# Kernel tuning notes

Hardware: AMD Instinct MI355X
Metric: run time of the kernel (lower is better)

Reference implementation:

```python
import jax, jax.numpy as jnp
import numpy as np

N = 100000   # nodes
E = 1600000  # edges (avg degree 16)
F_IN = 50    # dataset.num_features
C = 32       # dataset.num_classes == hidden == out channels


def setup_inputs() -> dict:
    key = jax.random.key(0)
    ks = jax.random.split(key, 12)
    x = jax.random.normal(ks[0], (N, F_IN), dtype=jnp.float32)
    edge_index = jax.random.randint(ks[1], (2, E), 0, N, dtype=jnp.int64)
    dims = [(F_IN, C), (C, C), (C, C)]
    inp = {"x": x, "edge_index": edge_index}
    for i, (din, dout) in enumerate(dims, start=1):
        s = 1.0 / np.sqrt(din)
        inp[f"Wl{i}"] = jax.random.uniform(ks[2 + 3 * (i - 1)], (din, dout), jnp.float32, -s, s)
        inp[f"bl{i}"] = jax.random.uniform(ks[3 + 3 * (i - 1)], (dout,), jnp.float32, -s, s)
        inp[f"Wr{i}"] = jax.random.uniform(ks[4 + 3 * (i - 1)], (din, dout), jnp.float32, -s, s)
    return inp


def _sage_conv(x, src, dst, Wl, bl, Wr):
    # message = x[src]; scatter-max into dst; lin_l(agg) + lin_r(x)
    msg = x[src]                                      # [E, d_in]
    agg = jax.ops.segment_max(msg, dst, num_segments=N)
    agg = jnp.where(jnp.isfinite(agg), agg, jnp.zeros((), agg.dtype))  # empty segments -> 0
    return agg @ Wl + bl + x @ Wr


def reference(x, edge_index, Wl1, bl1, Wr1, Wl2, bl2, Wr2, Wl3, bl3, Wr3):
    src, dst = edge_index[0], edge_index[1]
    h = jax.nn.relu(_sage_conv(x, src, dst, Wl1, bl1, Wr1))
    h = jax.nn.relu(_sage_conv(h, src, dst, Wl2, bl2, Wr2))
    h = _sage_conv(h, src, dst, Wl3, bl3, Wr3)
    return jax.nn.log_softmax(h, axis=1)
```

## Files before the change

### kernel.cpp

```cpp
#include <hip/hip_runtime.h>
#include <math.h>

#define NN 100000
#define CD 32
#define NPB 4

#define B1N ((NN + 255) >> 8)
#define EPB_A 2048

typedef unsigned int   uint32;
typedef unsigned short ushort16;

__device__ __forceinline__ ushort16 f2b(float f) {
    uint32 u = __float_as_uint(f);
    u = (u + 0x7FFFu + ((u >> 16) & 1u)) >> 16;
    return (ushort16)u;
}
__device__ __forceinline__ float b2f_lo(uint32 u) { return __uint_as_float(u << 16); }
__device__ __forceinline__ float b2f_hi(uint32 u) { return __uint_as_float(u & 0xFFFF0000u); }

__device__ __forceinline__ uint32 pkmax(uint32 a, uint32 b) {
    uint32 d;
    asm("v_pk_max_u16 %0, %1, %2" : "=v"(d) : "v"(a), "v"(b));
    return d;
}
__device__ __forceinline__ uint32 key16(float f) {
    uint32 b = (uint32)f2b(f);
    return b ^ ((__float_as_uint(f) >> 31) ? 0xFFFFu : 0x8000u);
}
__device__ __forceinline__ uint32 dec_pk(uint32 k) {
    uint32 m = (~k >> 15) & 0x00010001u;
    uint32 X = 0x80008000u | ((m << 15) - m);
    return k ^ X;
}

__device__ __forceinline__ int edge_is64(const void* edge) {
    const long long* p = (const long long*)edge;
    int lane = threadIdx.x & 63;
    int bad = 0;
    for (int i = lane; i < 512; i += 64) {
        long long v = p[i];
        if (v < 0 || v >= NN) bad = 1;
    }
    unsigned long long anybad = __ballot(bad);
    return (anybad == 0ULL) ? 1 : 0;
}

__device__ __forceinline__ int load_idx(const void* edge, int i, int is64) {
    if (is64) return (int)((const long long*)edge)[i];
    return ((const int*)edge)[i];
}

__global__ __launch_bounds__(256) void cvt_hist_kernel(const float* __restrict__ x,
                                                       uint32* __restrict__ xb,
                                                       const void* edge, int E,
                                                       int* __restrict__ hist,
                                                       int nblkA) {
    __shared__ int lh[B1N];
    const int t = threadIdx.x;
    if ((int)blockIdx.x < nblkA) {
        const int is64 = edge_is64(edge);
        for (int b = t; b < B1N; b += 256) lh[b] = 0;
        __syncthreads();
        const int e0 = blockIdx.x * EPB_A + t;
#pragma unroll
        for (int k = 0; k < 8; ++k) {
            int e = e0 + k * 256;
            if (e < E) {
                int d = load_idx(edge, E + e, is64);
                atomicAdd(&lh[d >> 8], 1);
            }
        }
        __syncthreads();
        int* gh = hist + (size_t)blockIdx.x * B1N;
        for (int b = t; b < B1N; b += 256) gh[b] = lh[b];
    } else {
        const int tt = (blockIdx.x - nblkA) * 256 + t;
        if (tt >= NN * 32) return;
        const int n = tt >> 5;
        const int c = tt & 31;
        if (c >= 25) { xb[tt] = 0; return; }
        float2 v = *(const float2*)&x[n * 50 + 2 * c];
        xb[tt] = key16(v.x) | (key16(v.y) << 16);
    }
}

__global__ __launch_bounds__(256) void scanA_kernel(int* __restrict__ hist,
                                                    int nblk,
                                                    int* __restrict__ binTotal) {
    __shared__ int ts[256];
    const int bin = blockIdx.x;
    const int t = threadIdx.x;
    const int base = t * 4;
    int v0 = (base + 0 < nblk) ? hist[(size_t)(base + 0) * B1N + bin] : 0;
    int v1 = (base + 1 < nblk) ? hist[(size_t)(base + 1) * B1N + bin] : 0;
    int v2 = (base + 2 < nblk) ? hist[(size_t)(base + 2) * B1N + bin] : 0;
    int v3 = (base + 3 < nblk) ? hist[(size_t)(base + 3) * B1N + bin] : 0;
    const int s = v0 + v1 + v2 + v3;
    ts[t] = s;
    __syncthreads();
    for (int off = 1; off < 256; off <<= 1) {
        int u = (t >= off) ? ts[t - off] : 0;
        __syncthreads();
        ts[t] += u;
        __syncthreads();
    }
    int e = ts[t] - s;
    if (base + 0 < nblk) { hist[(size_t)(base + 0) * B1N + bin] = e; e += v0; }
    if (base + 1 < nblk) { hist[(size_t)(base + 1) * B1N + bin] = e; e += v1; }
    if (base + 2 < nblk) { hist[(size_t)(base + 2) * B1N + bin] = e; e += v2; }
    if (base + 3 < nblk) { hist[(size_t)(base + 3) * B1N + bin] = e; e += v3; }
    if (t == 255) binTotal[bin] = ts[255];
}

__device__ __forceinline__ void scan_bins_lds(const int* __restrict__ binTotal,
                                              int* ts, int* lbase) {
    const int t = threadIdx.x;
    const int base = t * 2;
    const int v0 = (base + 0 < B1N) ? binTotal[base + 0] : 0;
    const int v1 = (base + 1 < B1N) ? binTotal[base + 1] : 0;
    const int s = v0 + v1;
    ts[t] = s;
    __syncthreads();
    for (int off = 1; off < 256; off <<= 1) {
        int u = (t >= off) ? ts[t - off] : 0;
        __syncthreads();
        ts[t] += u;
        __syncthreads();
    }
    const int e = ts[t] - s;
    if (base + 0 < B1N) lbase[base + 0] = e;
    if (base + 1 < B1N) lbase[base + 1] = e + v0;
    if (t == 255) lbase[B1N] = ts[255];
    __syncthreads();
}

__global__ __launch_bounds__(256) void scatter_kernel(const void* edge, int E,
                                                      const int* __restrict__ hist,
                                                      const int* __restrict__ binTotal,
                                                      uint32* __restrict__ bucketed) {
    __shared__ int ts[256];
    __shared__ int lbase[B1N + 1];
    __shared__ int cur[B1N];
    const int is64 = edge_is64(edge);
    const int t = threadIdx.x;
    scan_bins_lds(binTotal, ts, lbase);
    const int* gh = hist + (size_t)blockIdx.x * B1N;
    for (int b = t; b < B1N; b += 256) cur[b] = lbase[b] + gh[b];
    __syncthreads();
    const int e0 = blockIdx.x * EPB_A + t;
#pragma unroll
    for (int k = 0; k < 8; ++k) {
        int e = e0 + k * 256;
        if (e < E) {
            int s = load_idx(edge, e, is64);
            int d = load_idx(edge, E + e, is64);
            int pos = atomicAdd(&cur[d >> 8], 1);
            bucketed[pos] = (uint32)s | ((uint32)(d & 255) << 17);
        }
    }
}

__global__ __launch_bounds__(256) void bucket_kernel(const uint32* __restrict__ bucketed,
                                                     const int* __restrict__ binTotal,
                                                     int* __restrict__ offsets,
                                                     int* __restrict__ csr_src) {
    __shared__ int ts[256];
    __shared__ int lbase[B1N + 1];
    __shared__ int h[256];
    __shared__ int sc[256];
    __shared__ int cur[256];
    const int bkt = blockIdx.x;
    const int t = threadIdx.x;
    scan_bins_lds(binTotal, ts, lbase);
    const int start = lbase[bkt];
    const int end   = lbase[bkt + 1];
    h[t] = 0;
    __syncthreads();
    for (int i = start + t; i < end; i += 256)
        atomicAdd(&h[bucketed[i] >> 17], 1);
    __syncthreads();
    const int v = h[t];
    sc[t] = v;
    __syncthreads();
    for (int off = 1; off < 256; off <<= 1) {
        int u = (t >= off) ? sc[t - off] : 0;
        __syncthreads();
        sc[t] += u;
        __syncthreads();
    }
    const int excl = sc[t] - v;
    const int node = bkt * 256 + t;
    if (node < NN) offsets[node] = start + excl;
    cur[t] = start + excl;
    __syncthreads();
    for (int i = start + t; i < end; i += 256) {
        uint32 p = bucketed[i];
        int pos = atomicAdd(&cur[p >> 17], 1);
        csr_src[pos] = (int)(p & 0x1FFFFu);
    }
    if (bkt == B1N - 1 && t == 0) offsets[NN] = end;
}


__device__ __forceinline__ void g50_window(uint32* a_, int sidx, int mm,
                                           const char* hbase, uint32 joff,
                                           int p, int lb) {
    int k = p;
    for (; k + 14 < mm; k += 16) {
        const int kh = lb + (k >> 1);
#pragma unroll
        for (int kk = 0; kk < 8; ++kk) {
            int s = __shfl(sidx, kh + kk);
            uint32 u = *(const uint32*)(hbase + ((((uint32)s) << 7) | joff));
            a_[kk] = pkmax(a_[kk], u);
        }
    }
    for (; k + 6 < mm; k += 8) {
        const int kh = lb + (k >> 1);
#pragma unroll
        for (int kk = 0; kk < 4; ++kk) {
            int s = __shfl(sidx, kh + kk);
            uint32 u = *(const uint32*)(hbase + ((((uint32)s) << 7) | joff));
            a_[kk] = pkmax(a_[kk], u);
        }
    }
    for (; k < mm; k += 2) {
        int s = __shfl(sidx, lb + (k >> 1));
        uint32 u = *(const uint32*)(hbase + ((((uint32)s) << 7) | joff));
        a_[0] = pkmax(a_[0], u);
    }
}

__global__ void gather50_kernel(const uint32* __restrict__ hb,
                                const int* __restrict__ offsets,
                                const int* __restrict__ csr_src,
                                uint32* __restrict__ aggB) {
    const int tid  = threadIdx.x;
    const int g    = tid >> 6;
    const int lane = tid & 63;
    const int p    = lane >> 5;
    const int j    = lane & 31;
    const int n0   = (blockIdx.x * NPB + g) * 2;
    if (n0 >= NN) return;
    const int n1   = n0 + 1;
    const bool has1 = (n1 < NN);

    const int beg0 = offsets[n0];
    const int end0 = offsets[n0 + 1];
    const int beg1 = has1 ? offsets[n1] : 0;
    const int end1 = has1 ? offsets[n1 + 1] : 0;
    const char* hbase = (const char*)hb;
    const uint32 joff = (uint32)(j << 2);
    const int lb = p << 5;
    const int myidx = 2 * j + p;

    uint32 a_[8], b_[8];
#pragma unroll
    for (int k = 0; k < 8; ++k) { a_[k] = 0; b_[k] = 0; }

    const int d0 = end0 - beg0, d1 = end1 - beg1;
    const int mm0 = d0 < 64 ? d0 : 64;
    const int mm1 = d1 < 64 ? d1 : 64;
    int sidx0 = 0, sidx1 = 0;
    if (myidx < mm0) sidx0 = csr_src[beg0 + myidx];
    if (myidx < mm1) sidx1 = csr_src[beg1 + myidx];
    g50_window(a_, sidx0, mm0, hbase, joff, p, lb);
    g50_window(b_, sidx1, mm1, hbase, joff, p, lb);
    for (int ib = beg0 + 64; ib < end0; ib += 64) {
        const int rem = end0 - ib;
        const int mm = rem < 64 ? rem : 64;
        int s = (myidx < mm) ? csr_src[ib + myidx] : 0;
        g50_window(a_, s, mm, hbase, joff, p, lb);
    }
    for (int ib = beg1 + 64; ib < end1; ib += 64) {
        const int rem = end1 - ib;
        const int mm = rem < 64 ? rem : 64;
        int s = (myidx < mm) ? csr_src[ib + myidx] : 0;
        g50_window(b_, s, mm, hbase, joff, p, lb);
    }

#pragma unroll
    for (int off2 = 4; off2 > 0; off2 >>= 1)
#pragma unroll
        for (int k = 0; k < off2; ++k) {
            a_[k] = pkmax(a_[k], a_[k + off2]);
            b_[k] = pkmax(b_[k], b_[k + off2]);
        }
    uint32 r0 = a_[0], r1 = b_[0];
    r0 = pkmax(r0, (uint32)__shfl_xor((int)r0, 32));
    r1 = pkmax(r1, (uint32)__shfl_xor((int)r1, 32));
    if (p == 0 && j < 25) {
        aggB[(size_t)n0 * 32 + j] = (beg0 == end0) ? 0x80008000u : r0;
        if (has1)
            aggB[(size_t)n1 * 32 + j] = (beg1 == end1) ? 0x80008000u : r1;
    }
}

__device__ __forceinline__ void g32_window(uint32* a_, int sidx, int mm,
                                           const char* hbase, uint32 coff,
                                           int e, int lb) {
    int k = e;
    for (; k + 12 < mm; k += 16) {
        const int m = lb + (k >> 2);
        int s0 = __shfl(sidx, m);
        int s1 = __shfl(sidx, m + 1);
        int s2 = __shfl(sidx, m + 2);
        int s3 = __shfl(sidx, m + 3);
        uint32 u0 = *(const uint32*)(hbase + ((((uint32)s0) << 6) | coff));
        uint32 u1 = *(const uint32*)(hbase + ((((uint32)s1) << 6) | coff));
        uint32 u2 = *(const uint32*)(hbase + ((((uint32)s2) << 6) | coff));
        uint32 u3 = *(const uint32*)(hbase + ((((uint32)s3) << 6) | coff));
        a_[0] = pkmax(a_[0], u0); a_[1] = pkmax(a_[1], u1);
        a_[2] = pkmax(a_[2], u2); a_[3] = pkmax(a_[3], u3);
    }
    for (; k < mm; k += 4) {
        int s = __shfl(sidx, lb + (k >> 2));
        uint32 u = *(const uint32*)(hbase + ((((uint32)s) << 6) | coff));
        a_[0] = pkmax(a_[0], u);
    }
}

__global__ void gather32_kernel(const uint32* __restrict__ hb,
                                const int* __restrict__ offsets,
                                const int* __restrict__ csr_src,
                                uint32* __restrict__ aggB) {
    const int tid  = threadIdx.x;
    const int g    = tid >> 6;
    const int lane = tid & 63;
    const int e    = lane >> 4;
    const int c    = lane & 15;
    const int n0   = (blockIdx.x * NPB + g) * 2;
    if (n0 >= NN) return;
    const int n1   = n0 + 1;
    const bool has1 = (n1 < NN);

    const int beg0 = offsets[n0];
    const int end0 = offsets[n0 + 1];
    const int beg1 = has1 ? offsets[n1] : 0;
    const int end1 = has1 ? offsets[n1 + 1] : 0;
    const char* hbase = (const char*)hb;
    const uint32 coff = (uint32)(c << 2);
    const int lb = e << 4;
    const int myidx = 4 * c + e;

    uint32 a_[4] = {0, 0, 0, 0};
    uint32 b_[4] = {0, 0, 0, 0};

    const int d0 = end0 - beg0, d1 = end1 - beg1;
    const int mm0 = d0 < 64 ? d0 : 64;
    const int mm1 = d1 < 64 ? d1 : 64;
    int sidx0 = 0, sidx1 = 0;
    if (myidx < mm0) sidx0 = csr_src[beg0 + myidx];
    if (myidx < mm1) sidx1 = csr_src[beg1 + myidx];
    g32_window(a_, sidx0, mm0, hbase, coff, e, lb);
    g32_window(b_, sidx1, mm1, hbase, coff, e, lb);
    for (int ib = beg0 + 64; ib < end0; ib += 64) {
        const int rem = end0 - ib;
        const int mm = rem < 64 ? rem : 64;
        int s = (myidx < mm) ? csr_src[ib + myidx] : 0;
        g32_window(a_, s, mm, hbase, coff, e, lb);
    }
    for (int ib = beg1 + 64; ib < end1; ib += 64) {
        const int rem = end1 - ib;
        const int mm = rem < 64 ? rem : 64;
        int s = (myidx < mm) ? csr_src[ib + myidx] : 0;
        g32_window(b_, s, mm, hbase, coff, e, lb);
    }

    uint32 r0 = pkmax(pkmax(a_[0], a_[1]), pkmax(a_[2], a_[3]));
    uint32 r1 = pkmax(pkmax(b_[0], b_[1]), pkmax(b_[2], b_[3]));
    r0 = pkmax(r0, (uint32)__shfl_xor((int)r0, 16));
    r0 = pkmax(r0, (uint32)__shfl_xor((int)r0, 32));
    r1 = pkmax(r1, (uint32)__shfl_xor((int)r1, 16));
    r1 = pkmax(r1, (uint32)__shfl_xor((int)r1, 32));
    if (lane < 16) {
        aggB[(size_t)n0 * 16 + lane] = (beg0 == end0) ? 0x80008000u : r0;
        if (has1)
            aggB[(size_t)n1 * 16 + lane] = (beg1 == end1) ? 0x80008000u : r1;
    }
}

template <int DIN, int ASTR, int HSTR, int OSTR, int MODE>
__global__ void dense_kernel(const uint32* __restrict__ aggB,
                             const uint32* __restrict__ hB,
                             const float* __restrict__ Wl,
                             const float* __restrict__ bl,
                             const float* __restrict__ Wr,
                             void* __restrict__ out_v) {
    const int n = blockIdx.x * blockDim.x + threadIdx.x;
    if (n >= NN) return;

    float acc[CD];
#pragma unroll
    for (int j = 0; j < CD; ++j) acc[j] = bl[j];

    {
        const uint32* row = aggB + (size_t)n * ASTR;
        for (int c = 0; c < DIN / 4; ++c) {
            uint2 u = *(const uint2*)&row[c * 2];
            u.x = dec_pk(u.x); u.y = dec_pk(u.y);
            float d0 = b2f_lo(u.x), d1 = b2f_hi(u.x);
            float d2 = b2f_lo(u.y), d3 = b2f_hi(u.y);
            const float* w = Wl + c * 4 * CD;
#pragma unroll
            for (int j = 0; j < CD; ++j)
                acc[j] += d0 * w[j] + d1 * w[CD + j] + d2 * w[2 * CD + j] + d3 * w[3 * CD + j];
        }
        if (DIN % 4) {
            uint32 u = dec_pk(row[(DIN / 4) * 2]);
            float d0 = b2f_lo(u), d1 = b2f_hi(u);
            const float* w = Wl + (DIN - 2) * CD;
#pragma unroll
            for (int j = 0; j < CD; ++j)
                acc[j] += d0 * w[j] + d1 * w[CD + j];
        }
    }
    {
        const uint32* row = hB + (size_t)n * HSTR;
        for (int c = 0; c < DIN / 4; ++c) {
            uint2 u = *(const uint2*)&row[c * 2];
            u.x = dec_pk(u.x); u.y = dec_pk(u.y);
            float d0 = b2f_lo(u.x), d1 = b2f_hi(u.x);
            float d2 = b2f_lo(u.y), d3 = b2f_hi(u.y);
            const float* w = Wr + c * 4 * CD;
#pragma unroll
            for (int j = 0; j < CD; ++j)
                acc[j] += d0 * w[j] + d1 * w[CD + j] + d2 * w[2 * CD + j] + d3 * w[3 * CD + j];
        }
        if (DIN % 4) {
            uint32 u = dec_pk(row[(DIN / 4) * 2]);
            float d0 = b2f_lo(u), d1 = b2f_hi(u);
            const float* w = Wr + (DIN - 2) * CD;
#pragma unroll
            for (int j = 0; j < CD; ++j)
                acc[j] += d0 * w[j] + d1 * w[CD + j];
        }
    }

    if (MODE == 0) {
        uint32* orow = (uint32*)out_v + (size_t)n * OSTR;
#pragma unroll
        for (int c = 0; c < CD / 2; ++c) {
            float a0 = fmaxf(acc[2 * c],     0.0f);
            float a1 = fmaxf(acc[2 * c + 1], 0.0f);
            orow[c] = ((uint32)f2b(a0) | ((uint32)f2b(a1) << 16)) | 0x80008000u;
        }
    } else {
        float m = acc[0];
#pragma unroll
        for (int j = 1; j < CD; ++j) m = fmaxf(m, acc[j]);
        float s = 0.0f;
#pragma unroll
        for (int j = 0; j < CD; ++j) s += expf(acc[j] - m);
        const float lse = m + logf(s);
        float* orow = (float*)out_v + (size_t)n * CD;
#pragma unroll
        for (int j = 0; j < CD; ++j) orow[j] = acc[j] - lse;
    }
}

extern "C" void kernel_launch(void* const* d_in, const int* in_sizes, int n_in,
                              void* d_out, int out_size, void* d_ws, size_t ws_size,
                              hipStream_t stream) {
    const float* x    = (const float*)d_in[0];
    const void*  edge = d_in[1];
    const float* Wl1 = (const float*)d_in[2];
    const float* bl1 = (const float*)d_in[3];
    const float* Wr1 = (const float*)d_in[4];
    const float* Wl2 = (const float*)d_in[5];
    const float* bl2 = (const float*)d_in[6];
    const float* Wr2 = (const float*)d_in[7];
    const float* Wl3 = (const float*)d_in[8];
    const float* bl3 = (const float*)d_in[9];
    const float* Wr3 = (const float*)d_in[10];

    const int E = in_sizes[1] / 2;

    char* ws = (char*)d_ws;
    size_t off = 0;
    auto carve = [&](size_t bytes) {
        void* p = ws + off;
        off = (off + bytes + 255) & ~(size_t)255;
        return p;
    };
    int*    offsets   = (int*)   carve((size_t)(NN + 1) * 4);
    int*    binTotal  = (int*)   carve((size_t)B1N * 4);
    int*    csr_src   = (int*)   carve((size_t)E * 4);
    uint32* xb        = (uint32*)carve((size_t)NN * 32 * 4);
    uint32* h1b       = (uint32*)carve((size_t)NN * 16 * 4);
    (void)ws_size; (void)n_in; (void)out_size;

    uint32* bucketed = (uint32*)d_out;
    int*    hist     = (int*)((char*)d_out + (((size_t)E * 4 + 255) & ~(size_t)255));
    uint32* agg1 = (uint32*)d_out;
    uint32* agg2 = (uint32*)d_out;
    uint32* h2b  = xb;
    uint32* agg3 = h1b;

    const int nblkA = (E + EPB_A - 1) / EPB_A;
    const int cvtb  = (NN * 32 + 255) / 256;
    cvt_hist_kernel<<<nblkA + cvtb, 256, 0, stream>>>(x, xb, edge, E, hist, nblkA);
    scanA_kernel<<<B1N, 256, 0, stream>>>(hist, nblkA, binTotal);
    scatter_kernel<<<nblkA, 256, 0, stream>>>(edge, E, hist, binTotal, bucketed);
    bucket_kernel<<<B1N, 256, 0, stream>>>(bucketed, binTotal, offsets, csr_src);

    const int gb = (NN + NPB * 2 - 1) / (NPB * 2);
    const int db = (NN + 255) / 256;

    gather50_kernel<<<gb, 256, 0, stream>>>(xb, offsets, csr_src, agg1);
    dense_kernel<50, 32, 32, 16, 0><<<db, 256, 0, stream>>>(agg1, xb, Wl1, bl1, Wr1, h1b);
    gather32_kernel<<<gb, 256, 0, stream>>>(h1b, offsets, csr_src, agg2);
    dense_kernel<32, 16, 16, 16, 0><<<db, 256, 0, stream>>>(agg2, h1b, Wl2, bl2, Wr2, h2b);
    gather32_kernel<<<gb, 256, 0, stream>>>(h2b, offsets, csr_src, agg3);
    dense_kernel<32, 16, 16, 0, 2><<<db, 256, 0, stream>>>(agg3, h2b, Wl3, bl3, Wr3, d_out);
}
```

Measured before the change: 289.2 us.

## Fuse all stages into one persistent cooperative kernel with grid syncs

Replaces the ten separate kernel launches (histogram, scans, scatter, bucket, three gather and three dense stages) with one cooperative persistent kernel. Each stage loops over virtual blocks and stages are separated by grid.sync(). The goal is to remove launch gaps and inter-kernel drain/fill bubbles. The cost is grid-sync overhead, occupancy reduced by the combined LDS and register footprint, and grid-stride looping that may load-balance worse than native launches.

```diff
diff --git a/kernel.cpp b/kernel.cpp
--- a/kernel.cpp
+++ b/kernel.cpp
@@ -1,9 +1,13 @@
 #include <hip/hip_runtime.h>
+#include <hip/hip_cooperative_groups.h>
 #include <math.h>
+
+namespace cg = cooperative_groups;
 
 #define NN 100000
 #define CD 32
 #define NPB 4
+#define G_NPW 2
 
 #define B1N ((NN + 255) >> 8)
 #define EPB_A 2048
@@ -51,157 +55,17 @@
     return ((const int*)edge)[i];
 }
 
-__global__ __launch_bounds__(256) void cvt_hist_kernel(const float* __restrict__ x,
-                                                       uint32* __restrict__ xb,
-                                                       const void* edge, int E,
-                                                       int* __restrict__ hist,
-                                                       int nblkA) {
-    __shared__ int lh[B1N];
-    const int t = threadIdx.x;
-    if ((int)blockIdx.x < nblkA) {
-        const int is64 = edge_is64(edge);
-        for (int b = t; b < B1N; b += 256) lh[b] = 0;
-        __syncthreads();
-        const int e0 = blockIdx.x * EPB_A + t;
-#pragma unroll
-        for (int k = 0; k < 8; ++k) {
-            int e = e0 + k * 256;
-            if (e < E) {
-                int d = load_idx(edge, E + e, is64);
-                atomicAdd(&lh[d >> 8], 1);
-            }
-        }
-        __syncthreads();
-        int* gh = hist + (size_t)blockIdx.x * B1N;
-        for (int b = t; b < B1N; b += 256) gh[b] = lh[b];
-    } else {
-        const int tt = (blockIdx.x - nblkA) * 256 + t;
-        if (tt >= NN * 32) return;
-        const int n = tt >> 5;
-        const int c = tt & 31;
-        if (c >= 25) { xb[tt] = 0; return; }
-        float2 v = *(const float2*)&x[n * 50 + 2 * c];
-        xb[tt] = key16(v.x) | (key16(v.y) << 16);
-    }
-}
-
-__global__ __launch_bounds__(256) void scanA_kernel(int* __restrict__ hist,
-                                                    int nblk,
-                                                    int* __restrict__ binTotal) {
-    __shared__ int ts[256];
-    const int bin = blockIdx.x;
-    const int t = threadIdx.x;
-    const int base = t * 4;
-    int v0 = (base + 0 < nblk) ? hist[(size_t)(base + 0) * B1N + bin] : 0;
-    int v1 = (base + 1 < nblk) ? hist[(size_t)(base + 1) * B1N + bin] : 0;
-    int v2 = (base + 2 < nblk) ? hist[(size_t)(base + 2) * B1N + bin] : 0;
-    int v3 = (base + 3 < nblk) ? hist[(size_t)(base + 3) * B1N + bin] : 0;
-    const int s = v0 + v1 + v2 + v3;
-    ts[t] = s;
-    __syncthreads();
-    for (int off = 1; off < 256; off <<= 1) {
-        int u = (t >= off) ? ts[t - off] : 0;
-        __syncthreads();
-        ts[t] += u;
-        __syncthreads();
-    }
-    int e = ts[t] - s;
-    if (base + 0 < nblk) { hist[(size_t)(base + 0) * B1N + bin] = e; e += v0; }
-    if (base + 1 < nblk) { hist[(size_t)(base + 1) * B1N + bin] = e; e += v1; }
-    if (base + 2 < nblk) { hist[(size_t)(base + 2) * B1N + bin] = e; e += v2; }
-    if (base + 3 < nblk) { hist[(size_t)(base + 3) * B1N + bin] = e; e += v3; }
-    if (t == 255) binTotal[bin] = ts[255];
-}
-
-__device__ __forceinline__ void scan_bins_lds(const int* __restrict__ binTotal,
-                                              int* ts, int* lbase) {
-    const int t = threadIdx.x;
-    const int base = t * 2;
-    const int v0 = (base + 0 < B1N) ? binTotal[base + 0] : 0;
-    const int v1 = (base + 1 < B1N) ? binTotal[base + 1] : 0;
-    const int s = v0 + v1;
-    ts[t] = s;
-    __syncthreads();
-    for (int off = 1; off < 256; off <<= 1) {
-        int u = (t >= off) ? ts[t - off] : 0;
-        __syncthreads();
-        ts[t] += u;
-        __syncthreads();
-    }
-    const int e = ts[t] - s;
-    if (base + 0 < B1N) lbase[base + 0] = e;
-    if (base + 1 < B1N) lbase[base + 1] = e + v0;
-    if (t == 255) lbase[B1N] = ts[255];
-    __syncthreads();
-}
-
-__global__ __launch_bounds__(256) void scatter_kernel(const void* edge, int E,
-                                                      const int* __restrict__ hist,
-                                                      const int* __restrict__ binTotal,
-                                                      uint32* __restrict__ bucketed) {
-    __shared__ int ts[256];
-    __shared__ int lbase[B1N + 1];
-    __shared__ int cur[B1N];
-    const int is64 = edge_is64(edge);
-    const int t = threadIdx.x;
-    scan_bins_lds(binTotal, ts, lbase);
-    const int* gh = hist + (size_t)blockIdx.x * B1N;
-    for (int b = t; b < B1N; b += 256) cur[b] = lbase[b] + gh[b];
-    __syncthreads();
-    const int e0 = blockIdx.x * EPB_A + t;
-#pragma unroll
-    for (int k = 0; k < 8; ++k) {
-        int e = e0 + k * 256;
-        if (e < E) {
-            int s = load_idx(edge, e, is64);
-            int d = load_idx(edge, E + e, is64);
-            int pos = atomicAdd(&cur[d >> 8], 1);
-            bucketed[pos] = (uint32)s | ((uint32)(d & 255) << 17);
-        }
-    }
-}
-
-__global__ __launch_bounds__(256) void bucket_kernel(const uint32* __restrict__ bucketed,
-                                                     const int* __restrict__ binTotal,
-                                                     int* __restrict__ offsets,
-                                                     int* __restrict__ csr_src) {
-    __shared__ int ts[256];
-    __shared__ int lbase[B1N + 1];
-    __shared__ int h[256];
-    __shared__ int sc[256];
-    __shared__ int cur[256];
-    const int bkt = blockIdx.x;
-    const int t = threadIdx.x;
-    scan_bins_lds(binTotal, ts, lbase);
-    const int start = lbase[bkt];
-    const int end   = lbase[bkt + 1];
-    h[t] = 0;
-    __syncthreads();
-    for (int i = start + t; i < end; i += 256)
-        atomicAdd(&h[bucketed[i] >> 17], 1);
-    __syncthreads();
-    const int v = h[t];
-    sc[t] = v;
-    __syncthreads();
-    for (int off = 1; off < 256; off <<= 1) {
-        int u = (t >= off) ? sc[t - off] : 0;
-        __syncthreads();
-        sc[t] += u;
-        __syncthreads();
-    }
-    const int excl = sc[t] - v;
-    const int node = bkt * 256 + t;
-    if (node < NN) offsets[node] = start + excl;
-    cur[t] = start + excl;
-    __syncthreads();
-    for (int i = start + t; i < end; i += 256) {
-        uint32 p = bucketed[i];
-        int pos = atomicAdd(&cur[p >> 17], 1);
-        csr_src[pos] = (int)(p & 0x1FFFFu);
-    }
-    if (bkt == B1N - 1 && t == 0) offsets[NN] = end;
-}
-
+
+struct MegaArgs {
+    const float* x;
+    const void*  edge;
+    int E, nblkA, cvtb, gb, db;
+    const float *Wl1, *bl1, *Wr1, *Wl2, *bl2, *Wr2, *Wl3, *bl3, *Wr3;
+    uint32* xb; int* hist; int* binTotal; int* offsets; int* csr_src;
+    const uint32* bucketed_r; uint32* bucketed_w;
+    uint32* agg1; uint32* h1b; uint32* agg2; uint32* h2b; uint32* agg3;
+    float* outf;
+};
 
 __device__ __forceinline__ void g50_window(uint32* a_, int sidx, int mm,
                                            const char* hbase, uint32 joff,
@@ -232,16 +96,16 @@
     }
 }
 
-__global__ void gather50_kernel(const uint32* __restrict__ hb,
-                                const int* __restrict__ offsets,
-                                const int* __restrict__ csr_src,
-                                uint32* __restrict__ aggB) {
+__device__ __forceinline__ void gather50_body(int vb, const uint32* hb,
+                                              const int* offsets,
+                                              const int* csr_src,
+                                              uint32* aggB) {
     const int tid  = threadIdx.x;
     const int g    = tid >> 6;
     const int lane = tid & 63;
     const int p    = lane >> 5;
     const int j    = lane & 31;
-    const int n0   = (blockIdx.x * NPB + g) * 2;
+    const int n0   = (vb * NPB + g) * 2;
     if (n0 >= NN) return;
     const int n1   = n0 + 1;
     const bool has1 = (n1 < NN);
@@ -279,7 +143,6 @@
         int s = (myidx < mm) ? csr_src[ib + myidx] : 0;
         g50_window(b_, s, mm, hbase, joff, p, lb);
     }
-
 #pragma unroll
     for (int off2 = 4; off2 > 0; off2 >>= 1)
 #pragma unroll
@@ -321,16 +184,16 @@
     }
 }
 
-__global__ void gather32_kernel(const uint32* __restrict__ hb,
-                                const int* __restrict__ offsets,
-                                const int* __restrict__ csr_src,
-                                uint32* __restrict__ aggB) {
+__device__ __forceinline__ void gather32_body(int vb, const uint32* hb,
+                                              const int* offsets,
+                                              const int* csr_src,
+                                              uint32* aggB) {
     const int tid  = threadIdx.x;
     const int g    = tid >> 6;
     const int lane = tid & 63;
     const int e    = lane >> 4;
     const int c    = lane & 15;
-    const int n0   = (blockIdx.x * NPB + g) * 2;
+    const int n0   = (vb * NPB + g) * 2;
     if (n0 >= NN) return;
     const int n1   = n0 + 1;
     const bool has1 = (n1 < NN);
@@ -382,13 +245,11 @@
 }
 
 template <int DIN, int ASTR, int HSTR, int OSTR, int MODE>
-__global__ void dense_kernel(const uint32* __restrict__ aggB,
-                             const uint32* __restrict__ hB,
-                             const float* __restrict__ Wl,
-                             const float* __restrict__ bl,
-                             const float* __restrict__ Wr,
-                             void* __restrict__ out_v) {
-    const int n = blockIdx.x * blockDim.x + threadIdx.x;
+__device__ __forceinline__ void dense_body(int vb, const uint32* aggB,
+                                           const uint32* hB,
+                                           const float* Wl, const float* bl,
+                                           const float* Wr, void* out_v) {
+    const int n = vb * 256 + threadIdx.x;
     if (n >= NN) return;
 
     float acc[CD];
@@ -460,20 +321,180 @@
     }
 }
 
+__global__ void mega_kernel(MegaArgs A) {
+    cg::grid_group grid = cg::this_grid();
+    const int NB  = gridDim.x;
+    const int bid = blockIdx.x;
+    const int t   = threadIdx.x;
+
+    __shared__ int lh[B1N];
+    __shared__ int ts[256];
+    __shared__ int lbase[B1N + 1];
+    __shared__ int hh[256];
+    __shared__ int sc[256];
+    __shared__ int cur[B1N];
+
+    const int is64 = edge_is64(A.edge);
+
+    for (int vb = bid; vb < A.nblkA + A.cvtb; vb += NB) {
+        if (vb < A.nblkA) {
+            for (int b = t; b < B1N; b += 256) lh[b] = 0;
+            __syncthreads();
+            const int e0 = vb * EPB_A + t;
+#pragma unroll
+            for (int k = 0; k < 8; ++k) {
+                int e = e0 + k * 256;
+                if (e < A.E) {
+                    int d = load_idx(A.edge, A.E + e, is64);
+                    atomicAdd(&lh[d >> 8], 1);
+                }
+            }
+            __syncthreads();
+            int* gh = A.hist + (size_t)vb * B1N;
+            for (int b = t; b < B1N; b += 256) gh[b] = lh[b];
+            __syncthreads();
+        } else {
+            const int tt = (vb - A.nblkA) * 256 + t;
+            if (tt < NN * 32) {
+                const int n = tt >> 5;
+                const int c = tt & 31;
+                if (c >= 25) A.xb[tt] = 0;
+                else {
+                    float2 v = *(const float2*)&A.x[n * 50 + 2 * c];
+                    A.xb[tt] = key16(v.x) | (key16(v.y) << 16);
+                }
+            }
+        }
+    }
+    grid.sync();
+
+    for (int vb = bid; vb < B1N; vb += NB) {
+        const int bin = vb;
+        const int base = t * 4;
+        int v0 = (base + 0 < A.nblkA) ? A.hist[(size_t)(base + 0) * B1N + bin] : 0;
+        int v1 = (base + 1 < A.nblkA) ? A.hist[(size_t)(base + 1) * B1N + bin] : 0;
+        int v2 = (base + 2 < A.nblkA) ? A.hist[(size_t)(base + 2) * B1N + bin] : 0;
+        int v3 = (base + 3 < A.nblkA) ? A.hist[(size_t)(base + 3) * B1N + bin] : 0;
+        const int s = v0 + v1 + v2 + v3;
+        ts[t] = s;
+        __syncthreads();
+        for (int off = 1; off < 256; off <<= 1) {
+            int u = (t >= off) ? ts[t - off] : 0;
+            __syncthreads();
+            ts[t] += u;
+            __syncthreads();
+        }
+        int e = ts[t] - s;
+        if (base + 0 < A.nblkA) { A.hist[(size_t)(base + 0) * B1N + bin] = e; e += v0; }
+        if (base + 1 < A.nblkA) { A.hist[(size_t)(base + 1) * B1N + bin] = e; e += v1; }
+        if (base + 2 < A.nblkA) { A.hist[(size_t)(base + 2) * B1N + bin] = e; e += v2; }
+        if (base + 3 < A.nblkA) { A.hist[(size_t)(base + 3) * B1N + bin] = e; e += v3; }
+        if (t == 255) A.binTotal[bin] = ts[255];
+        __syncthreads();
+    }
+    grid.sync();
+
+    auto scan_bins = [&]() {
+        const int base = t * 2;
+        const int v0 = (base + 0 < B1N) ? A.binTotal[base + 0] : 0;
+        const int v1 = (base + 1 < B1N) ? A.binTotal[base + 1] : 0;
+        const int s = v0 + v1;
+        ts[t] = s;
+        __syncthreads();
+        for (int off = 1; off < 256; off <<= 1) {
+            int u = (t >= off) ? ts[t - off] : 0;
+            __syncthreads();
+            ts[t] += u;
+            __syncthreads();
+        }
+        const int e = ts[t] - s;
+        if (base + 0 < B1N) lbase[base + 0] = e;
+        if (base + 1 < B1N) lbase[base + 1] = e + v0;
+        if (t == 255) lbase[B1N] = ts[255];
+        __syncthreads();
+    };
+
+    scan_bins();
+    for (int vb = bid; vb < A.nblkA; vb += NB) {
+        const int* gh = A.hist + (size_t)vb * B1N;
+        for (int b = t; b < B1N; b += 256) cur[b] = lbase[b] + gh[b];
+        __syncthreads();
+        const int e0 = vb * EPB_A + t;
+#pragma unroll
+        for (int k = 0; k < 8; ++k) {
+            int e = e0 + k * 256;
+            if (e < A.E) {
+                int s = load_idx(A.edge, e, is64);
+                int d = load_idx(A.edge, A.E + e, is64);
+                int pos = atomicAdd(&cur[d >> 8], 1);
+                A.bucketed_w[pos] = (uint32)s | ((uint32)(d & 255) << 17);
+            }
+        }
+        __syncthreads();
+    }
+    grid.sync();
+
+    for (int vb = bid; vb < B1N; vb += NB) {
+        const int start = lbase[vb];
+        const int end   = lbase[vb + 1];
+        hh[t] = 0;
+        __syncthreads();
+        for (int i = start + t; i < end; i += 256)
+            atomicAdd(&hh[A.bucketed_r[i] >> 17], 1);
+        __syncthreads();
+        const int v = hh[t];
+        sc[t] = v;
+        __syncthreads();
+        for (int off = 1; off < 256; off <<= 1) {
+            int u = (t >= off) ? sc[t - off] : 0;
+            __syncthreads();
+            sc[t] += u;
+            __syncthreads();
+        }
+        const int excl = sc[t] - v;
+        const int node = vb * 256 + t;
+        if (node < NN) A.offsets[node] = start + excl;
+        cur[t] = start + excl;
+        __syncthreads();
+        for (int i = start + t; i < end; i += 256) {
+            uint32 p = A.bucketed_r[i];
+            int pos = atomicAdd(&cur[p >> 17], 1);
+            A.csr_src[pos] = (int)(p & 0x1FFFFu);
+        }
+        if (vb == B1N - 1 && t == 0) A.offsets[NN] = end;
+        __syncthreads();
+    }
+    grid.sync();
+
+    for (int vb = bid; vb < A.gb; vb += NB)
+        gather50_body(vb, A.xb, A.offsets, A.csr_src, A.agg1);
+    grid.sync();
+
+    for (int vb = bid; vb < A.db; vb += NB)
+        dense_body<50, 32, 32, 16, 0>(vb, A.agg1, A.xb, A.Wl1, A.bl1, A.Wr1, A.h1b);
+    grid.sync();
+
+    for (int vb = bid; vb < A.gb; vb += NB)
+        gather32_body(vb, A.h1b, A.offsets, A.csr_src, A.agg2);
+    grid.sync();
+
+    for (int vb = bid; vb < A.db; vb += NB)
+        dense_body<32, 16, 16, 16, 0>(vb, A.agg2, A.h1b, A.Wl2, A.bl2, A.Wr2, A.h2b);
+    grid.sync();
+
+    for (int vb = bid; vb < A.gb; vb += NB)
+        gather32_body(vb, A.h2b, A.offsets, A.csr_src, A.agg3);
+    grid.sync();
+
+    for (int vb = bid; vb < A.db; vb += NB)
+        dense_body<32, 16, 16, 0, 2>(vb, A.agg3, A.h2b, A.Wl3, A.bl3, A.Wr3, A.outf);
+}
+
 extern "C" void kernel_launch(void* const* d_in, const int* in_sizes, int n_in,
                               void* d_out, int out_size, void* d_ws, size_t ws_size,
                               hipStream_t stream) {
     const float* x    = (const float*)d_in[0];
     const void*  edge = d_in[1];
-    const float* Wl1 = (const float*)d_in[2];
-    const float* bl1 = (const float*)d_in[3];
-    const float* Wr1 = (const float*)d_in[4];
-    const float* Wl2 = (const float*)d_in[5];
-    const float* bl2 = (const float*)d_in[6];
-    const float* Wr2 = (const float*)d_in[7];
-    const float* Wl3 = (const float*)d_in[8];
-    const float* bl3 = (const float*)d_in[9];
-    const float* Wr3 = (const float*)d_in[10];
 
     const int E = in_sizes[1] / 2;
 
@@ -493,25 +514,39 @@
 
     uint32* bucketed = (uint32*)d_out;
     int*    hist     = (int*)((char*)d_out + (((size_t)E * 4 + 255) & ~(size_t)255));
-    uint32* agg1 = (uint32*)d_out;
-    uint32* agg2 = (uint32*)d_out;
-    uint32* h2b  = xb;
-    uint32* agg3 = h1b;
-
-    const int nblkA = (E + EPB_A - 1) / EPB_A;
-    const int cvtb  = (NN * 32 + 255) / 256;
-    cvt_hist_kernel<<<nblkA + cvtb, 256, 0, stream>>>(x, xb, edge, E, hist, nblkA);
-    scanA_kernel<<<B1N, 256, 0, stream>>>(hist, nblkA, binTotal);
-    scatter_kernel<<<nblkA, 256, 0, stream>>>(edge, E, hist, binTotal, bucketed);
-    bucket_kernel<<<B1N, 256, 0, stream>>>(bucketed, binTotal, offsets, csr_src);
-
-    const int gb = (NN + NPB * 2 - 1) / (NPB * 2);
-    const int db = (NN + 255) / 256;
-
-    gather50_kernel<<<gb, 256, 0, stream>>>(xb, offsets, csr_src, agg1);
-    dense_kernel<50, 32, 32, 16, 0><<<db, 256, 0, stream>>>(agg1, xb, Wl1, bl1, Wr1, h1b);
-    gather32_kernel<<<gb, 256, 0, stream>>>(h1b, offsets, csr_src, agg2);
-    dense_kernel<32, 16, 16, 16, 0><<<db, 256, 0, stream>>>(agg2, h1b, Wl2, bl2, Wr2, h2b);
-    gather32_kernel<<<gb, 256, 0, stream>>>(h2b, offsets, csr_src, agg3);
-    dense_kernel<32, 16, 16, 0, 2><<<db, 256, 0, stream>>>(agg3, h2b, Wl3, bl3, Wr3, d_out);
-}
+
+    MegaArgs a;
+    a.x = x; a.edge = edge; a.E = E;
+    a.nblkA = (E + EPB_A - 1) / EPB_A;
+    a.cvtb  = (NN * 32 + 255) / 256;
+    a.gb    = (NN + NPB * G_NPW - 1) / (NPB * G_NPW);
+    a.db    = (NN + 255) / 256;
+    a.Wl1 = (const float*)d_in[2];  a.bl1 = (const float*)d_in[3];
+    a.Wr1 = (const float*)d_in[4];
+    a.Wl2 = (const float*)d_in[5];  a.bl2 = (const float*)d_in[6];
+    a.Wr2 = (const float*)d_in[7];
+    a.Wl3 = (const float*)d_in[8];  a.bl3 = (const float*)d_in[9];
+    a.Wr3 = (const float*)d_in[10];
+    a.xb = xb; a.hist = hist; a.binTotal = binTotal;
+    a.offsets = offsets; a.csr_src = csr_src;
+    a.bucketed_r = bucketed; a.bucketed_w = bucketed;
+    a.agg1 = (uint32*)d_out;
+    a.h1b  = h1b;
+    a.agg2 = (uint32*)d_out;
+    a.h2b  = xb;
+    a.agg3 = h1b;
+    a.outf = (float*)d_out;
+
+    static int gridBlocks = 0;
+    if (gridBlocks == 0) {
+        int nb = 0;
+        hipOccupancyMaxActiveBlocksPerMultiprocessor(&nb, (const void*)mega_kernel, 256, 0);
+        if (nb < 1) nb = 1;
+        gridBlocks = nb * 256;
+        if (gridBlocks > 2048) gridBlocks = 2048;
+    }
+
+    void* kargs[] = { &a };
+    hipLaunchCooperativeKernel((const void*)mega_kernel, dim3(gridBlocks),
+                               dim3(256), kargs, 0, stream);
+}
```

Result: slower. 1.110 ms (+283.9%).
